# Optimization experiments

Measured on AMD Instinct MI355X. Metric: run time of the kernel, lower is better.

Reference implementation:

```python
import jax, jax.numpy as jnp
import numpy as np

N_NODES = 20000
N_EDGES = 320000
D_IN = 256      # n_source_nodes (input feature dim)
HEADS = 4
HEAD_DIM = 64   # n_target_nodes // heads
D_OUT = HEADS * HEAD_DIM  # n_target_nodes = 256
EDGE_DIM = 1


def setup_inputs() -> dict:
    key = jax.random.key(0)
    ks = jax.random.split(key, 12)
    s = 0.05
    return {
        "x": jax.random.normal(ks[0], (N_NODES, D_IN), jnp.float32),
        "edge_index": jax.random.randint(ks[1], (2, N_EDGES), 0, N_NODES, jnp.int64),
        "edge_attr": jax.random.normal(ks[2], (N_EDGES, EDGE_DIM), jnp.float32),
        # TransformerConv params (weights stored [in, out]; PyG Linear defaults: q/k/v have bias, edge lin has no bias, skip lin has bias)
        "Wq": jax.random.normal(ks[3], (D_IN, D_OUT), jnp.float32) * s,
        "bq": jnp.zeros((D_OUT,), jnp.float32),
        "Wk": jax.random.normal(ks[4], (D_IN, D_OUT), jnp.float32) * s,
        "bk": jnp.zeros((D_OUT,), jnp.float32),
        "Wv": jax.random.normal(ks[5], (D_IN, D_OUT), jnp.float32) * s,
        "bv": jnp.zeros((D_OUT,), jnp.float32),
        "We": jax.random.normal(ks[6], (EDGE_DIM, D_OUT), jnp.float32) * s,
        "Wskip": jax.random.normal(ks[7], (D_IN, D_OUT), jnp.float32) * s,
        "bskip": jnp.zeros((D_OUT,), jnp.float32),
        # GraphNorm params
        "gn_weight": jnp.ones((D_OUT,), jnp.float32),
        "gn_bias": jnp.zeros((D_OUT,), jnp.float32),
        "gn_mean_scale": jnp.ones((D_OUT,), jnp.float32),
    }


def reference(x, edge_index, edge_attr, Wq, bq, Wk, bk, Wv, bv, We, Wskip, bskip, gn_weight, gn_bias, gn_mean_scale):
    N = x.shape[0]
    src, dst = edge_index[0], edge_index[1]  # message flows src -> dst (source_to_target)

    q = (x @ Wq + bq).reshape(N, HEADS, HEAD_DIM)
    k = (x @ Wk + bk).reshape(N, HEADS, HEAD_DIM)
    v = (x @ Wv + bv).reshape(N, HEADS, HEAD_DIM)
    e = (edge_attr @ We).reshape(-1, HEADS, HEAD_DIM)  # [E, H, C]

    k_j = k[src] + e                                   # [E, H, C]
    alpha = jnp.einsum('ehc,ehc->eh', q[dst], k_j) / jnp.sqrt(jnp.float32(HEAD_DIM))

    # segment softmax over edges sharing the same target node
    a_max = jax.ops.segment_max(alpha, dst, num_segments=N)[dst]
    a_exp = jnp.exp(alpha - a_max)
    a_sum = jax.ops.segment_sum(a_exp, dst, num_segments=N)[dst]
    att = a_exp / (a_sum + 1e-16)                      # [E, H]

    msg = (v[src] + e) * att[..., None]                # [E, H, C]
    out = jax.ops.segment_sum(msg, dst, num_segments=N).reshape(N, D_OUT)
    out = out + x @ Wskip + bskip                      # root/skip connection (beta=False)

    # GraphNorm (single graph): weight*(x - alpha*mean)/sqrt(var+eps) + bias
    mean = out.mean(axis=0)
    centered = out - gn_mean_scale * mean
    var = jnp.mean(centered * centered, axis=0)
    out = gn_weight * centered * jax.lax.rsqrt(var + 1e-5) + gn_bias

    out = jax.nn.relu(out)
    xt = out.T @ out                                   # [D_OUT, D_OUT]
    xt_min, xt_max = jnp.min(xt), jnp.max(xt)
    return (xt - xt_min) / (xt_max - xt_min + 1e-8)
```

## Files before the change

kernel.cpp:

```cpp
#include <hip/hip_runtime.h>
#include <math.h>

#define N_NODES 20000
#define N_EDGES 320000
#define SK 20480
#define APAD 80

typedef short short8 __attribute__((ext_vector_type(8)));
typedef float f32x4 __attribute__((ext_vector_type(4)));

static __device__ __forceinline__ unsigned short f2bf(float f) {
    unsigned int u = __float_as_uint(f);
    u = (u + 0x7FFF + ((u >> 16) & 1)) >> 16;
    return (unsigned short)u;
}
static __device__ __forceinline__ float b2f(unsigned short u) {
    return __uint_as_float((unsigned int)u << 16);
}
static __device__ __forceinline__ float blo(unsigned int u) {
    return __uint_as_float(u << 16);
}
static __device__ __forceinline__ float bhi(unsigned int u) {
    return __uint_as_float(u & 0xFFFF0000u);
}

__global__ __launch_bounds__(256) void prep_k(const float* __restrict__ x,
                                              unsigned short* __restrict__ xb,
                                              const float* __restrict__ Wq,
                                              const float* __restrict__ Wk,
                                              const float* __restrict__ Wv,
                                              const float* __restrict__ Wsk,
                                              const float* __restrict__ bq,
                                              const float* __restrict__ bk,
                                              const float* __restrict__ bv,
                                              const float* __restrict__ bsk,
                                              unsigned short* __restrict__ wT,
                                              float* __restrict__ bias_all,
                                              const int* __restrict__ dst,
                                              int* __restrict__ deg)
{
    const int b = blockIdx.x;
    const int tid = threadIdx.x;
    if (b < 2500) {
        const size_t base = ((size_t)b * 256 + tid) * 8;
        const float4 f0 = *(const float4*)(x + base);
        const float4 f1 = *(const float4*)(x + base + 4);
        ushort4 u0, u1;
        u0.x = f2bf(f0.x); u0.y = f2bf(f0.y); u0.z = f2bf(f0.z); u0.w = f2bf(f0.w);
        u1.x = f2bf(f1.x); u1.y = f2bf(f1.y); u1.z = f2bf(f1.z); u1.w = f2bf(f1.w);
        *(ushort4*)(xb + base) = u0;
        *(ushort4*)(xb + base + 4) = u1;
    } else if (b < 3524) {
        const int bb = b - 2500;
        const int wi = bb >> 8, n = bb & 255;
        const float* W = (wi == 0) ? Wq : (wi == 1) ? Wk : (wi == 2) ? Wv : Wsk;
        wT[(size_t)bb * 256 + tid] = f2bf(W[(size_t)tid * 256 + n]);
        if (tid == 0) {
            const float* bv_ = (wi == 0) ? bq : (wi == 1) ? bk : (wi == 2) ? bv : bsk;
            bias_all[bb] = bv_[n];
        }
    } else {
        const int e = (b - 3524) * 256 + tid;
        if (e < N_EDGES) atomicAdd(&deg[dst[e]], 1);
    }
}

__global__ __launch_bounds__(256, 4) void gemm_qkvs(const unsigned short* __restrict__ xb,
                                                    const unsigned short* __restrict__ wT,
                                                    const float* __restrict__ bias_all,
                                                    unsigned short* __restrict__ qb,
                                                    unsigned short* __restrict__ kvb,
                                                    float* __restrict__ ob)
{
    __shared__ __align__(16) unsigned short As[(128 + 128) * APAD];
    unsigned short* Bs = As + 128 * APAD;
    float* stage = (float*)As;

    const int tid  = threadIdx.x;
    const int lane = tid & 63;
    const int w    = tid >> 6;
    const int wm = w >> 1, wn = w & 1;
    const int row0 = blockIdx.x * 128;
    const int by   = blockIdx.y;
    const int wsel = by >> 1;
    const int ar = tid >> 1, ak = (tid & 1) * 32;
    const int fr = lane & 15, fk = (lane >> 4) * 8, lg = lane >> 4;

    f32x4 acc[4][4] = {};

    for (int k0 = 0; k0 < 256; k0 += 64) {
        int gr = row0 + ar; gr = gr < N_NODES ? gr : N_NODES - 1;
        const unsigned short* ap = xb + (size_t)gr * 256 + k0 + ak;
        const uint4 a0 = *(const uint4*)ap;
        const uint4 a1 = *(const uint4*)(ap + 8);
        const uint4 a2 = *(const uint4*)(ap + 16);
        const uint4 a3 = *(const uint4*)(ap + 24);
        const unsigned short* bp = wT + (size_t)(by * 128 + ar) * 256 + k0 + ak;
        const uint4 b0 = *(const uint4*)bp;
        const uint4 b1 = *(const uint4*)(bp + 8);
        const uint4 b2 = *(const uint4*)(bp + 16);
        const uint4 b3 = *(const uint4*)(bp + 24);
        __syncthreads();
        unsigned short* asp = &As[ar * APAD + ak];
        *(uint4*)asp        = a0;
        *(uint4*)(asp + 8)  = a1;
        *(uint4*)(asp + 16) = a2;
        *(uint4*)(asp + 24) = a3;
        unsigned short* bsp = &Bs[ar * APAD + ak];
        *(uint4*)bsp        = b0;
        *(uint4*)(bsp + 8)  = b1;
        *(uint4*)(bsp + 16) = b2;
        *(uint4*)(bsp + 24) = b3;
        __syncthreads();
#pragma unroll
        for (int ks = 0; ks < 2; ++ks) {
            short8 af[4], bf[4];
#pragma unroll
            for (int m = 0; m < 4; ++m)
                af[m] = *(const short8*)&As[(wm * 64 + m * 16 + fr) * APAD + ks * 32 + fk];
#pragma unroll
            for (int n = 0; n < 4; ++n)
                bf[n] = *(const short8*)&Bs[(wn * 64 + n * 16 + fr) * APAD + ks * 32 + fk];
#pragma unroll
            for (int m = 0; m < 4; ++m)
#pragma unroll
                for (int n = 0; n < 4; ++n)
                    acc[m][n] = __builtin_amdgcn_mfma_f32_16x16x32_bf16(af[m], bf[n], acc[m][n], 0, 0, 0);
        }
    }
    __syncthreads();

    float badd[4];
#pragma unroll
    for (int n = 0; n < 4; ++n) badd[n] = bias_all[by * 128 + wn * 64 + n * 16 + fr];

    float* st = stage + w * 1024;
    const int chalf = by & 1;
#pragma unroll
    for (int m = 0; m < 4; ++m) {
#pragma unroll
        for (int n = 0; n < 4; ++n)
#pragma unroll
            for (int r = 0; r < 4; ++r)
                st[(lg * 4 + r) * 64 + n * 16 + fr] = acc[m][n][r] + badd[n];
#pragma unroll
        for (int it = 0; it < 4; ++it) {
            const int lrow = it * 4 + lg;
            const f32x4 c4 = *(const f32x4*)&st[lrow * 64 + fr * 4];
            const int grow = row0 + wm * 64 + m * 16 + lrow;
            if (grow < N_NODES) {
                const int colin = chalf * 128 + wn * 64 + fr * 4;
                if (wsel == 3) {
                    float4 o; o.x = c4[0]; o.y = c4[1]; o.z = c4[2]; o.w = c4[3];
                    *(float4*)(ob + (size_t)grow * 256 + colin) = o;
                } else {
                    ushort4 u;
                    u.x = f2bf(c4[0]); u.y = f2bf(c4[1]); u.z = f2bf(c4[2]); u.w = f2bf(c4[3]);
                    if (wsel == 0) {
                        *(ushort4*)(qb + (size_t)grow * 256 + colin) = u;
                    } else {
                        const int c = chalf * 32 + wn * 16 + fr;
                        const size_t kvidx = (size_t)grow * 512 + c * 8 + (wsel == 1 ? 0 : 4);
                        *(ushort4*)(kvb + kvidx) = u;
                    }
                }
            }
        }
    }
}

__global__ __launch_bounds__(1024) void scan_k(const int* __restrict__ deg,
                                               int* __restrict__ row_start)
{
    __shared__ int sdeg[20480];
    const int tid = threadIdx.x;
    const int lane = tid & 63, wid = tid >> 6;
    const int CH = 20;
#pragma unroll
    for (int i = 0; i < 20; ++i) {
        const int idx = i * 1024 + tid;
        sdeg[idx] = (idx < N_NODES) ? deg[idx] : 0;
    }
    __syncthreads();
    const int base = tid * CH;
    int local[CH];
    int s = 0;
#pragma unroll
    for (int i = 0; i < CH; ++i) {
        local[i] = s;
        s += sdeg[base + i];
    }
    int v = s;
#pragma unroll
    for (int off = 1; off < 64; off <<= 1) {
        const int t = __shfl_up(v, off);
        if (lane >= off) v += t;
    }
    __shared__ int wsum[16];
    if (lane == 63) wsum[wid] = v;
    __syncthreads();
    if (tid == 0) {
        int r = 0;
        for (int i = 0; i < 16; ++i) { const int t = wsum[i]; wsum[i] = r; r += t; }
    }
    __syncthreads();
    const int excl = v - s + wsum[wid];
#pragma unroll
    for (int i = 0; i < CH; ++i) {
        const int idx = base + i;
        if (idx < N_NODES) row_start[idx] = excl + local[i];
    }
    if (tid == 1023) row_start[N_NODES] = excl + s;
}

__global__ void fill_csr(const int* __restrict__ dst, const int* __restrict__ src,
                         const float* __restrict__ ea,
                         const int* __restrict__ row_start,
                         int* __restrict__ cursor, int2* __restrict__ ekv)
{
    const int e = blockIdx.x * 256 + threadIdx.x;
    if (e < N_EDGES) {
        const int d = dst[e];
        const int p = atomicAdd(&cursor[d], 1);
        int2 pk;
        pk.x = src[e];
        pk.y = __float_as_int(ea[e]);
        ekv[row_start[d] + p] = pk;
    }
}

static __device__ __forceinline__ void edge_step(const uint4 kv, const float a,
                                                 const float4 qf, const float4 we4,
                                                 float& ssum, float& ax, float& ay,
                                                 float& az, float& aw)
{
    const float k0 = blo(kv.x), k1 = bhi(kv.x), k2 = blo(kv.y), k3 = bhi(kv.y);
    const float v0 = blo(kv.z), v1 = bhi(kv.z), v2 = blo(kv.w), v3 = bhi(kv.w);
    float p = qf.x * (k0 + a * we4.x) + qf.y * (k1 + a * we4.y)
            + qf.z * (k2 + a * we4.z) + qf.w * (k3 + a * we4.w);
    p += __shfl_xor(p, 1); p += __shfl_xor(p, 2);
    p += __shfl_xor(p, 4); p += __shfl_xor(p, 8);
    const float wgt = __expf(p * 0.125f);
    ssum += wgt;
    ax += wgt * (v0 + a * we4.x);
    ay += wgt * (v1 + a * we4.y);
    az += wgt * (v2 + a * we4.z);
    aw += wgt * (v3 + a * we4.w);
}

__global__ __launch_bounds__(256) void attn_k(const unsigned short* __restrict__ qb,
                                              const unsigned short* __restrict__ kvb,
                                              const float* __restrict__ We,
                                              const int* __restrict__ row_start,
                                              const int2* __restrict__ ekv,
                                              float* __restrict__ out)
{
    const int wid  = threadIdx.x >> 6;
    const int lane = threadIdx.x & 63;
    const int n = blockIdx.x * 4 + wid;
    if (n >= N_NODES) return;

    const ushort4 qv = *(const ushort4*)(qb + (size_t)n * 256 + lane * 4);
    float4 qf;
    qf.x = b2f(qv.x); qf.y = b2f(qv.y); qf.z = b2f(qv.z); qf.w = b2f(qv.w);
    const float4 we4 = *(const float4*)(We + lane * 4);
    const int rs = row_start[n], re = row_start[n + 1];
    const int lo8 = lane * 8;

    float ssum = 0.f;
    float ax = 0.f, ay = 0.f, az = 0.f, aw = 0.f;

    int s = rs;
    for (; s + 4 <= re; s += 4) {
        const int2 p0 = ekv[s],     p1 = ekv[s + 1];
        const int2 p2 = ekv[s + 2], p3 = ekv[s + 3];
        const int sn0 = ((unsigned)p0.x < N_NODES) ? p0.x : 0;
        const int sn1 = ((unsigned)p1.x < N_NODES) ? p1.x : 0;
        const int sn2 = ((unsigned)p2.x < N_NODES) ? p2.x : 0;
        const int sn3 = ((unsigned)p3.x < N_NODES) ? p3.x : 0;
        const uint4 kv0 = *(const uint4*)(kvb + (size_t)sn0 * 512 + lo8);
        const uint4 kv1 = *(const uint4*)(kvb + (size_t)sn1 * 512 + lo8);
        const uint4 kv2 = *(const uint4*)(kvb + (size_t)sn2 * 512 + lo8);
        const uint4 kv3 = *(const uint4*)(kvb + (size_t)sn3 * 512 + lo8);
        edge_step(kv0, __int_as_float(p0.y), qf, we4, ssum, ax, ay, az, aw);
        edge_step(kv1, __int_as_float(p1.y), qf, we4, ssum, ax, ay, az, aw);
        edge_step(kv2, __int_as_float(p2.y), qf, we4, ssum, ax, ay, az, aw);
        edge_step(kv3, __int_as_float(p3.y), qf, we4, ssum, ax, ay, az, aw);
    }
    for (; s < re; ++s) {
        const int2 p0 = ekv[s];
        const int sn0 = ((unsigned)p0.x < N_NODES) ? p0.x : 0;
        const uint4 kv0 = *(const uint4*)(kvb + (size_t)sn0 * 512 + lo8);
        edge_step(kv0, __int_as_float(p0.y), qf, we4, ssum, ax, ay, az, aw);
    }
    const float inv = 1.f / (ssum + 1e-16f);
    const float4 sk = *(const float4*)(out + (size_t)n * 256 + lane * 4);
    float4 o;
    o.x = ax * inv + sk.x;
    o.y = ay * inv + sk.y;
    o.z = az * inv + sk.z;
    o.w = aw * inv + sk.w;
    *(float4*)(out + (size_t)n * 256 + lane * 4) = o;
}

__global__ __launch_bounds__(256) void gn_stats_k(const float* __restrict__ out,
                                                  float* __restrict__ gstats)
{
    const int c = threadIdx.x;
    float s = 0.f, s2 = 0.f;
    for (int r = blockIdx.x; r < N_NODES; r += gridDim.x) {
        const float vv = out[(size_t)r * 256 + c];
        s += vv; s2 += vv * vv;
    }
    atomicAdd(&gstats[c], s);
    atomicAdd(&gstats[256 + c], s2);
}

__global__ __launch_bounds__(256) void norm_relu_T(const float* __restrict__ ob,
                                                   const float* __restrict__ gstats,
                                                   const float* __restrict__ gw,
                                                   const float* __restrict__ gb,
                                                   const float* __restrict__ gms,
                                                   unsigned short* __restrict__ obT)
{
    __shared__ unsigned short tile[256][72];
    __shared__ float smu[256], swi[256], sbd[256];
    const int t = threadIdx.x;
    const int r0 = blockIdx.x * 64;
    {
        const float invN = 1.f / (float)N_NODES;
        const float mean = gstats[t] * invN;
        const float exx  = gstats[256 + t] * invN;
        const float mu   = gms[t] * mean;
        const float var  = exx - 2.f * mu * mean + mu * mu;
        smu[t] = mu;
        swi[t] = gw[t] * rsqrtf(var + 1e-5f);
        sbd[t] = gb[t];
    }
    __syncthreads();
    const int rr = t >> 2;
    const int row = r0 + rr;
#pragma unroll
    for (int it = 0; it < 16; ++it) {
        const int col = it * 16 + (t & 3) * 4;
        float4 f = make_float4(0.f, 0.f, 0.f, 0.f);
        if (row < N_NODES) f = *(const float4*)(ob + (size_t)row * 256 + col);
        ushort4 u;
        if (row < N_NODES) {
            u.x = f2bf(fmaxf((f.x - smu[col + 0]) * swi[col + 0] + sbd[col + 0], 0.f));
            u.y = f2bf(fmaxf((f.y - smu[col + 1]) * swi[col + 1] + sbd[col + 1], 0.f));
            u.z = f2bf(fmaxf((f.z - smu[col + 2]) * swi[col + 2] + sbd[col + 2], 0.f));
            u.w = f2bf(fmaxf((f.w - smu[col + 3]) * swi[col + 3] + sbd[col + 3], 0.f));
        } else { u.x = u.y = u.z = u.w = 0; }
        tile[col + 0][rr] = u.x;
        tile[col + 1][rr] = u.y;
        tile[col + 2][rr] = u.z;
        tile[col + 3][rr] = u.w;
    }
    __syncthreads();
#pragma unroll
    for (int it = 0; it < 8; ++it) {
        const int c = it * 32 + (t >> 3);
        const int part = t & 7;
        const uint4 x0 = *(const uint4*)&tile[c][part * 8];
        *(uint4*)(obT + (size_t)c * SK + r0 + part * 8) = x0;
    }
}

__global__ __launch_bounds__(256) void gram_k(const unsigned short* __restrict__ obT,
                                              float* __restrict__ xt)
{
    const int bi_l[10] = {0,0,0,0,1,1,1,2,2,3};
    const int bj_l[10] = {0,1,2,3,1,2,3,2,3,3};
    const int bi = bi_l[blockIdx.x], bj = bj_l[blockIdx.x];
    const int r0 = blockIdx.y * 1024;

    __shared__ __align__(16) unsigned short Ai[64 * 136];
    __shared__ __align__(16) unsigned short Aj[64 * 136];
    const int tid = threadIdx.x;
    const int lane = tid & 63;
    const int w = tid >> 6;
    const int wi = w >> 1, wj = w & 1;
    const int lr = tid >> 2, kseg = (tid & 3) * 32;
    const int fr = lane & 15, fk = (lane >> 4) * 8, lg = lane >> 4;

    f32x4 acc[2][2] = {};

    for (int kt = 0; kt < 1024; kt += 128) {
        uint4 ai[4], aj[4];
        const unsigned short* pa = obT + (size_t)(bi * 64 + lr) * SK + r0 + kt + kseg;
        const unsigned short* pb = obT + (size_t)(bj * 64 + lr) * SK + r0 + kt + kseg;
#pragma unroll
        for (int j = 0; j < 4; ++j) { ai[j] = *(const uint4*)(pa + 8 * j); aj[j] = *(const uint4*)(pb + 8 * j); }
        __syncthreads();
#pragma unroll
        for (int j = 0; j < 4; ++j) {
            *(uint4*)&Ai[lr * 136 + kseg + 8 * j] = ai[j];
            *(uint4*)&Aj[lr * 136 + kseg + 8 * j] = aj[j];
        }
        __syncthreads();
#pragma unroll
        for (int ks = 0; ks < 4; ++ks) {
            short8 af[2], bf[2];
#pragma unroll
            for (int m = 0; m < 2; ++m)
                af[m] = *(const short8*)&Ai[(wi * 32 + m * 16 + fr) * 136 + ks * 32 + fk];
#pragma unroll
            for (int n = 0; n < 2; ++n)
                bf[n] = *(const short8*)&Aj[(wj * 32 + n * 16 + fr) * 136 + ks * 32 + fk];
#pragma unroll
            for (int m = 0; m < 2; ++m)
#pragma unroll
                for (int n = 0; n < 2; ++n)
                    acc[m][n] = __builtin_amdgcn_mfma_f32_16x16x32_bf16(af[m], bf[n], acc[m][n], 0, 0, 0);
        }
    }
#pragma unroll
    for (int m = 0; m < 2; ++m)
#pragma unroll
        for (int n = 0; n < 2; ++n)
#pragma unroll
            for (int r = 0; r < 4; ++r)
                atomicAdd(&xt[(size_t)(bi * 64 + wi * 32 + m * 16 + lg * 4 + r) * 256
                              + bj * 64 + wj * 32 + n * 16 + fr], acc[m][n][r]);
}

__global__ __launch_bounds__(1024) void minmax_k(const float* __restrict__ xt,
                                                 float* __restrict__ mm)
{
    const int tid = threadIdx.x;
    float mn = 1e30f, mx = -1e30f;
    for (int i = tid; i < 65536; i += 1024) {
        const int r = i >> 8, c = i & 255;
        if ((r >> 6) <= (c >> 6)) {
            const float v = xt[i];
            mn = fminf(mn, v);
            mx = fmaxf(mx, v);
        }
    }
    for (int off = 1; off < 64; off <<= 1) {
        mn = fminf(mn, __shfl_xor(mn, off));
        mx = fmaxf(mx, __shfl_xor(mx, off));
    }
    __shared__ float smn[16], smx[16];
    const int w = tid >> 6;
    if ((tid & 63) == 0) { smn[w] = mn; smx[w] = mx; }
    __syncthreads();
    if (tid == 0) {
        for (int i = 1; i < 16; ++i) {
            mn = fminf(mn, smn[i]);
            mx = fmaxf(mx, smx[i]);
        }
        mm[0] = mn; mm[1] = mx;
    }
}

__global__ void finalize_k(const float* __restrict__ xt, const float* __restrict__ mm,
                           float* __restrict__ outp)
{
    const int i = blockIdx.x * 256 + threadIdx.x;
    const int r = i >> 8, c = i & 255;
    const float v = ((r >> 6) <= (c >> 6)) ? xt[i] : xt[c * 256 + r];
    const float mn = mm[0], mx = mm[1];
    const float inv = 1.f / (mx - mn + 1e-8f);
    outp[i] = (v - mn) * inv;
}

extern "C" void kernel_launch(void* const* d_in, const int* in_sizes, int n_in,
                              void* d_out, int out_size, void* d_ws, size_t ws_size,
                              hipStream_t stream)
{
    (void)in_sizes; (void)n_in; (void)out_size; (void)ws_size;
    const float* x   = (const float*)d_in[0];
    const int*   ei  = (const int*)d_in[1];
    const float* ea  = (const float*)d_in[2];
    const float* Wq  = (const float*)d_in[3];
    const float* bq  = (const float*)d_in[4];
    const float* Wk  = (const float*)d_in[5];
    const float* bk  = (const float*)d_in[6];
    const float* Wv  = (const float*)d_in[7];
    const float* bv  = (const float*)d_in[8];
    const float* We  = (const float*)d_in[9];
    const float* Wsk = (const float*)d_in[10];
    const float* bsk = (const float*)d_in[11];
    const float* gw  = (const float*)d_in[12];
    const float* gb  = (const float*)d_in[13];
    const float* gms = (const float*)d_in[14];
    float* outp = (float*)d_out;

    char* ws = (char*)d_ws;
    size_t off = 0;
    #define WS_ALLOC(nbytes) (ws + off); off = (off + (size_t)(nbytes) + 255) & ~(size_t)255
    unsigned short* xb  = (unsigned short*)WS_ALLOC((size_t)N_NODES * 256 * 2);
    unsigned short* wT  = (unsigned short*)WS_ALLOC((size_t)1024 * 256 * 2);
    float* bias_all     = (float*)WS_ALLOC(1024 * 4);
    unsigned short* qb  = (unsigned short*)WS_ALLOC((size_t)N_NODES * 256 * 2);
    unsigned short* kvb = (unsigned short*)WS_ALLOC((size_t)N_NODES * 512 * 2);
    float* ob           = (float*)WS_ALLOC((size_t)N_NODES * 256 * 4);
    const size_t zoff = off;
    int*   deg    = (int*)WS_ALLOC((size_t)N_NODES * 4);
    int*   cur    = (int*)WS_ALLOC((size_t)N_NODES * 4);
    float* gstats = (float*)WS_ALLOC(512 * 4);
    float* xt     = (float*)WS_ALLOC(65536 * 4);
    const size_t zbytes = off - zoff;
    int* row_start = (int*)WS_ALLOC((size_t)(N_NODES + 1) * 4);
    float* mm      = (float*)WS_ALLOC(2 * 4);
    #undef WS_ALLOC
    int2* ekv           = (int2*)xb;
    unsigned short* obT = (unsigned short*)xb;

    const int* srcv = ei;
    const int* dstv = ei + N_EDGES;

    hipMemsetAsync(ws + zoff, 0, zbytes, stream);

    prep_k<<<2500 + 1024 + 1250, 256, 0, stream>>>(x, xb, Wq, Wk, Wv, Wsk,
                                                   bq, bk, bv, bsk, wT, bias_all,
                                                   dstv, deg);

    gemm_qkvs<<<dim3((N_NODES + 127) / 128, 8), 256, 0, stream>>>(xb, wT, bias_all,
                                                                  qb, kvb, ob);

    scan_k<<<1, 1024, 0, stream>>>(deg, row_start);
    fill_csr<<<(N_EDGES + 255) / 256, 256, 0, stream>>>(dstv, srcv, ea, row_start, cur, ekv);

    attn_k<<<(N_NODES + 3) / 4, 256, 0, stream>>>(qb, kvb, We, row_start, ekv, ob);

    gn_stats_k<<<400, 256, 0, stream>>>(ob, gstats);
    norm_relu_T<<<320, 256, 0, stream>>>(ob, gstats, gw, gb, gms, obT);

    gram_k<<<dim3(10, 20), 256, 0, stream>>>(obT, xt);
    minmax_k<<<1, 1024, 0, stream>>>(xt, mm);
    finalize_k<<<256, 256, 0, stream>>>(xt, mm, outp);
}
```

Before: 219.3 us.

## Store skip/output buffer in bf16, split gram over more blocks, fuse minmax with finalize

The skip-connection/attention output buffer changes from fp32 to bf16, which halves its traffic through the GEMM epilogue, attn_k, gn_stats and norm_relu_T. gram_k now splits the node dimension into 512-row chunks over twice as many blocks and uses a larger LDS pitch. The separate min/max and finalize kernels are merged into one single-block kernel, which removes a launch. The trade-offs are extra bf16 rounding on the pre-norm activations, more atomic adds into xt, and a finalize step that now runs on only one block.

```diff
diff --git a/kernel.cpp b/kernel.cpp
--- a/kernel.cpp
+++ b/kernel.cpp
@@ -5,6 +5,7 @@
 #define N_EDGES 320000
 #define SK 20480
 #define APAD 80
+#define GPITCH 144
 
 typedef short short8 __attribute__((ext_vector_type(8)));
 typedef float f32x4 __attribute__((ext_vector_type(4)));
@@ -70,7 +71,7 @@
                                                     const float* __restrict__ bias_all,
                                                     unsigned short* __restrict__ qb,
                                                     unsigned short* __restrict__ kvb,
-                                                    float* __restrict__ ob)
+                                                    unsigned short* __restrict__ ob)
 {
     __shared__ __align__(16) unsigned short As[(128 + 128) * APAD];
     unsigned short* Bs = As + 128 * APAD;
@@ -150,19 +151,16 @@
             const int grow = row0 + wm * 64 + m * 16 + lrow;
             if (grow < N_NODES) {
                 const int colin = chalf * 128 + wn * 64 + fr * 4;
+                ushort4 u;
+                u.x = f2bf(c4[0]); u.y = f2bf(c4[1]); u.z = f2bf(c4[2]); u.w = f2bf(c4[3]);
                 if (wsel == 3) {
-                    float4 o; o.x = c4[0]; o.y = c4[1]; o.z = c4[2]; o.w = c4[3];
-                    *(float4*)(ob + (size_t)grow * 256 + colin) = o;
+                    *(ushort4*)(ob + (size_t)grow * 256 + colin) = u;
+                } else if (wsel == 0) {
+                    *(ushort4*)(qb + (size_t)grow * 256 + colin) = u;
                 } else {
-                    ushort4 u;
-                    u.x = f2bf(c4[0]); u.y = f2bf(c4[1]); u.z = f2bf(c4[2]); u.w = f2bf(c4[3]);
-                    if (wsel == 0) {
-                        *(ushort4*)(qb + (size_t)grow * 256 + colin) = u;
-                    } else {
-                        const int c = chalf * 32 + wn * 16 + fr;
-                        const size_t kvidx = (size_t)grow * 512 + c * 8 + (wsel == 1 ? 0 : 4);
-                        *(ushort4*)(kvb + kvidx) = u;
-                    }
+                    const int c = chalf * 32 + wn * 16 + fr;
+                    const size_t kvidx = (size_t)grow * 512 + c * 8 + (wsel == 1 ? 0 : 4);
+                    *(ushort4*)(kvb + kvidx) = u;
                 }
             }
         }
@@ -253,7 +251,7 @@
                                               const float* __restrict__ We,
                                               const int* __restrict__ row_start,
                                               const int2* __restrict__ ekv,
-                                              float* __restrict__ out)
+                                              unsigned short* __restrict__ out)
 {
     const int wid  = threadIdx.x >> 6;
     const int lane = threadIdx.x & 63;
@@ -294,29 +292,29 @@
         edge_step(kv0, __int_as_float(p0.y), qf, we4, ssum, ax, ay, az, aw);
     }
     const float inv = 1.f / (ssum + 1e-16f);
-    const float4 sk = *(const float4*)(out + (size_t)n * 256 + lane * 4);
-    float4 o;
-    o.x = ax * inv + sk.x;
-    o.y = ay * inv + sk.y;
-    o.z = az * inv + sk.z;
-    o.w = aw * inv + sk.w;
-    *(float4*)(out + (size_t)n * 256 + lane * 4) = o;
-}
-
-__global__ __launch_bounds__(256) void gn_stats_k(const float* __restrict__ out,
+    const ushort4 sk4 = *(const ushort4*)(out + (size_t)n * 256 + lane * 4);
+    ushort4 ou;
+    ou.x = f2bf(ax * inv + b2f(sk4.x));
+    ou.y = f2bf(ay * inv + b2f(sk4.y));
+    ou.z = f2bf(az * inv + b2f(sk4.z));
+    ou.w = f2bf(aw * inv + b2f(sk4.w));
+    *(ushort4*)(out + (size_t)n * 256 + lane * 4) = ou;
+}
+
+__global__ __launch_bounds__(256) void gn_stats_k(const unsigned short* __restrict__ out,
                                                   float* __restrict__ gstats)
 {
     const int c = threadIdx.x;
     float s = 0.f, s2 = 0.f;
     for (int r = blockIdx.x; r < N_NODES; r += gridDim.x) {
-        const float vv = out[(size_t)r * 256 + c];
+        const float vv = b2f(out[(size_t)r * 256 + c]);
         s += vv; s2 += vv * vv;
     }
     atomicAdd(&gstats[c], s);
     atomicAdd(&gstats[256 + c], s2);
 }
 
-__global__ __launch_bounds__(256) void norm_relu_T(const float* __restrict__ ob,
+__global__ __launch_bounds__(256) void norm_relu_T(const unsigned short* __restrict__ ob,
                                                    const float* __restrict__ gstats,
                                                    const float* __restrict__ gw,
                                                    const float* __restrict__ gb,
@@ -343,14 +341,13 @@
 #pragma unroll
     for (int it = 0; it < 16; ++it) {
         const int col = it * 16 + (t & 3) * 4;
-        float4 f = make_float4(0.f, 0.f, 0.f, 0.f);
-        if (row < N_NODES) f = *(const float4*)(ob + (size_t)row * 256 + col);
         ushort4 u;
         if (row < N_NODES) {
-            u.x = f2bf(fmaxf((f.x - smu[col + 0]) * swi[col + 0] + sbd[col + 0], 0.f));
-            u.y = f2bf(fmaxf((f.y - smu[col + 1]) * swi[col + 1] + sbd[col + 1], 0.f));
-            u.z = f2bf(fmaxf((f.z - smu[col + 2]) * swi[col + 2] + sbd[col + 2], 0.f));
-            u.w = f2bf(fmaxf((f.w - smu[col + 3]) * swi[col + 3] + sbd[col + 3], 0.f));
+            const ushort4 uv = *(const ushort4*)(ob + (size_t)row * 256 + col);
+            u.x = f2bf(fmaxf((b2f(uv.x) - smu[col + 0]) * swi[col + 0] + sbd[col + 0], 0.f));
+            u.y = f2bf(fmaxf((b2f(uv.y) - smu[col + 1]) * swi[col + 1] + sbd[col + 1], 0.f));
+            u.z = f2bf(fmaxf((b2f(uv.z) - smu[col + 2]) * swi[col + 2] + sbd[col + 2], 0.f));
+            u.w = f2bf(fmaxf((b2f(uv.w) - smu[col + 3]) * swi[col + 3] + sbd[col + 3], 0.f));
         } else { u.x = u.y = u.z = u.w = 0; }
         tile[col + 0][rr] = u.x;
         tile[col + 1][rr] = u.y;
@@ -373,10 +370,10 @@
     const int bi_l[10] = {0,0,0,0,1,1,1,2,2,3};
     const int bj_l[10] = {0,1,2,3,1,2,3,2,3,3};
     const int bi = bi_l[blockIdx.x], bj = bj_l[blockIdx.x];
-    const int r0 = blockIdx.y * 1024;
-
-    __shared__ __align__(16) unsigned short Ai[64 * 136];
-    __shared__ __align__(16) unsigned short Aj[64 * 136];
+    const int r0 = blockIdx.y * 512;
+
+    __shared__ __align__(16) unsigned short Ai[64 * GPITCH];
+    __shared__ __align__(16) unsigned short Aj[64 * GPITCH];
     const int tid = threadIdx.x;
     const int lane = tid & 63;
     const int w = tid >> 6;
@@ -386,7 +383,7 @@
 
     f32x4 acc[2][2] = {};
 
-    for (int kt = 0; kt < 1024; kt += 128) {
+    for (int kt = 0; kt < 512; kt += 128) {
         uint4 ai[4], aj[4];
         const unsigned short* pa = obT + (size_t)(bi * 64 + lr) * SK + r0 + kt + kseg;
         const unsigned short* pb = obT + (size_t)(bj * 64 + lr) * SK + r0 + kt + kseg;
@@ -395,8 +392,8 @@
         __syncthreads();
 #pragma unroll
         for (int j = 0; j < 4; ++j) {
-            *(uint4*)&Ai[lr * 136 + kseg + 8 * j] = ai[j];
-            *(uint4*)&Aj[lr * 136 + kseg + 8 * j] = aj[j];
+            *(uint4*)&Ai[lr * GPITCH + kseg + 8 * j] = ai[j];
+            *(uint4*)&Aj[lr * GPITCH + kseg + 8 * j] = aj[j];
         }
         __syncthreads();
 #pragma unroll
@@ -404,10 +401,10 @@
             short8 af[2], bf[2];
 #pragma unroll
             for (int m = 0; m < 2; ++m)
-                af[m] = *(const short8*)&Ai[(wi * 32 + m * 16 + fr) * 136 + ks * 32 + fk];
+                af[m] = *(const short8*)&Ai[(wi * 32 + m * 16 + fr) * GPITCH + ks * 32 + fk];
 #pragma unroll
             for (int n = 0; n < 2; ++n)
-                bf[n] = *(const short8*)&Aj[(wj * 32 + n * 16 + fr) * 136 + ks * 32 + fk];
+                bf[n] = *(const short8*)&Aj[(wj * 32 + n * 16 + fr) * GPITCH + ks * 32 + fk];
 #pragma unroll
             for (int m = 0; m < 2; ++m)
 #pragma unroll
@@ -425,8 +422,8 @@
                               + bj * 64 + wj * 32 + n * 16 + fr], acc[m][n][r]);
 }
 
-__global__ __launch_bounds__(1024) void minmax_k(const float* __restrict__ xt,
-                                                 float* __restrict__ mm)
+__global__ __launch_bounds__(1024) void minmax_fin_k(const float* __restrict__ xt,
+                                                     float* __restrict__ outp)
 {
     const int tid = threadIdx.x;
     float mn = 1e30f, mx = -1e30f;
@@ -443,6 +440,7 @@
         mx = fmaxf(mx, __shfl_xor(mx, off));
     }
     __shared__ float smn[16], smx[16];
+    __shared__ float fmn, fmx;
     const int w = tid >> 6;
     if ((tid & 63) == 0) { smn[w] = mn; smx[w] = mx; }
     __syncthreads();
@@ -451,19 +449,16 @@
             mn = fminf(mn, smn[i]);
             mx = fmaxf(mx, smx[i]);
         }
-        mm[0] = mn; mm[1] = mx;
-    }
-}
-
-__global__ void finalize_k(const float* __restrict__ xt, const float* __restrict__ mm,
-                           float* __restrict__ outp)
-{
-    const int i = blockIdx.x * 256 + threadIdx.x;
-    const int r = i >> 8, c = i & 255;
-    const float v = ((r >> 6) <= (c >> 6)) ? xt[i] : xt[c * 256 + r];
-    const float mn = mm[0], mx = mm[1];
-    const float inv = 1.f / (mx - mn + 1e-8f);
-    outp[i] = (v - mn) * inv;
+        fmn = mn; fmx = mx;
+    }
+    __syncthreads();
+    const float gmn = fmn;
+    const float inv = 1.f / (fmx - gmn + 1e-8f);
+    for (int i = tid; i < 65536; i += 1024) {
+        const int r = i >> 8, c = i & 255;
+        const float v = ((r >> 6) <= (c >> 6)) ? xt[i] : xt[c * 256 + r];
+        outp[i] = (v - gmn) * inv;
+    }
 }
 
 extern "C" void kernel_launch(void* const* d_in, const int* in_sizes, int n_in,
@@ -496,7 +491,7 @@
     float* bias_all     = (float*)WS_ALLOC(1024 * 4);
     unsigned short* qb  = (unsigned short*)WS_ALLOC((size_t)N_NODES * 256 * 2);
     unsigned short* kvb = (unsigned short*)WS_ALLOC((size_t)N_NODES * 512 * 2);
-    float* ob           = (float*)WS_ALLOC((size_t)N_NODES * 256 * 4);
+    unsigned short* ob  = (unsigned short*)WS_ALLOC((size_t)N_NODES * 256 * 2);
     const size_t zoff = off;
     int*   deg    = (int*)WS_ALLOC((size_t)N_NODES * 4);
     int*   cur    = (int*)WS_ALLOC((size_t)N_NODES * 4);
@@ -504,7 +499,6 @@
     float* xt     = (float*)WS_ALLOC(65536 * 4);
     const size_t zbytes = off - zoff;
     int* row_start = (int*)WS_ALLOC((size_t)(N_NODES + 1) * 4);
-    float* mm      = (float*)WS_ALLOC(2 * 4);
     #undef WS_ALLOC
     int2* ekv           = (int2*)xb;
     unsigned short* obT = (unsigned short*)xb;
@@ -529,7 +523,6 @@
     gn_stats_k<<<400, 256, 0, stream>>>(ob, gstats);
     norm_relu_T<<<320, 256, 0, stream>>>(ob, gstats, gw, gb, gms, obT);
 
-    gram_k<<<dim3(10, 20), 256, 0, stream>>>(obT, xt);
-    minmax_k<<<1, 1024, 0, stream>>>(xt, mm);
-    finalize_k<<<256, 256, 0, stream>>>(xt, mm, outp);
-}
+    gram_k<<<dim3(10, 40), 256, 0, stream>>>(obT, xt);
+    minmax_fin_k<<<1, 1024, 0, stream>>>(xt, outp);
+}
```

Result: slower. 225.9 us (+3.0%).
